# Kernel tuning notes

Hardware: AMD Instinct MI355X
Metric: run time of the kernel (lower is better)

Reference implementation:

```python
import jax, jax.numpy as jnp
import numpy as np

N_NODES = 20000
N_EDGES = 320000
NUM_GRAPHS = 64
IN_DIM = 256


def setup_inputs() -> dict:
    key = jax.random.key(0)
    ks = jax.random.split(key, 12)
    x = jax.random.normal(ks[0], (N_NODES, IN_DIM), dtype=jnp.float32)
    edge_index = jax.random.randint(ks[1], (2, N_EDGES), 0, N_NODES, dtype=jnp.int64)
    batch = jnp.sort(jax.random.randint(ks[2], (N_NODES,), 0, NUM_GRAPHS, dtype=jnp.int64))
    def glorot(k, shape):
        lim = float(np.sqrt(6.0 / (shape[0] + shape[1])))
        return jax.random.uniform(k, shape, dtype=jnp.float32, minval=-lim, maxval=lim)
    W1 = glorot(ks[3], (IN_DIM, 256)); b1 = jnp.zeros((256,), jnp.float32)
    W2 = glorot(ks[4], (256, 128));   b2 = jnp.zeros((128,), jnp.float32)
    Wl1 = glorot(ks[5], (128, 64));   bl1 = jnp.zeros((64,), jnp.float32)
    Wl2 = glorot(ks[6], (64, 1));     bl2 = jnp.zeros((1,), jnp.float32)
    return {"x": x, "edge_index": edge_index, "batch": batch,
            "W1": W1, "b1": b1, "W2": W2, "b2": b2,
            "Wl1": Wl1, "bl1": bl1, "Wl2": Wl2, "bl2": bl2}


def gcn_conv(x, src, dst, W, b, n_nodes):
    # PyG GCNConv: add self-loops, symmetric normalization D^-1/2 (A+I) D^-1/2,
    # linear transform first, then gather-scale-scatter aggregation, then bias.
    loop = jnp.arange(n_nodes, dtype=src.dtype)
    s = jnp.concatenate([src, loop])
    d = jnp.concatenate([dst, loop])
    deg = jax.ops.segment_sum(jnp.ones_like(d, dtype=x.dtype), d, num_segments=n_nodes)
    dinv = jnp.where(deg > 0, jax.lax.rsqrt(deg), 0.0)
    norm = dinv[s] * dinv[d]                         # [E+N]
    h = x @ W                                        # [N, out]
    msg = h[s] * norm[:, None]                       # [E+N, out]
    out = jax.ops.segment_sum(msg, d, num_segments=n_nodes)
    return out + b


def global_mean_pool(x, batch, num_graphs):
    sums = jax.ops.segment_sum(x, batch, num_segments=num_graphs)
    cnts = jax.ops.segment_sum(jnp.ones((x.shape[0],), x.dtype), batch, num_segments=num_graphs)
    return sums / jnp.maximum(cnts, 1.0)[:, None]


def reference(x, edge_index, batch, W1, b1, W2, b2, Wl1, bl1, Wl2, bl2):
    n = x.shape[0]
    src, dst = edge_index[0], edge_index[1]
    h = jax.nn.relu(gcn_conv(x, src, dst, W1, b1, n))   # dropout = identity (eval)
    h = jax.nn.relu(gcn_conv(h, src, dst, W2, b2, n))
    g = global_mean_pool(h, batch, NUM_GRAPHS)          # [G, 128]
    g = jax.nn.relu(g @ Wl1 + bl1)
    return jax.nn.sigmoid(g @ Wl2 + bl2)                # [G, 1]
```

## Files before the change

### kernel.cpp

```cpp
#include <hip/hip_runtime.h>
#include <hip/hip_bf16.h>
#include <math.h>

typedef __attribute__((ext_vector_type(8))) short bf16x8;
typedef __attribute__((ext_vector_type(4))) float f32x4;

__device__ __forceinline__ unsigned short f2bf(float f) {
    unsigned int u = __float_as_uint(f);
    unsigned int r = (u + 0x7FFFu + ((u >> 16) & 1u)) >> 16;
    return (unsigned short)r;
}
__device__ __forceinline__ float bf2f(unsigned short h) {
    return __uint_as_float(((unsigned int)h) << 16);
}
__device__ __forceinline__ unsigned char f2fp8(float v) {
    int p = __builtin_amdgcn_cvt_pk_fp8_f32(v, v, 0, false);
    return (unsigned char)(p & 0xff);
}
__device__ __forceinline__ unsigned int pk4fp8(float a, float b, float c, float d) {
    int p = __builtin_amdgcn_cvt_pk_fp8_f32(a, b, 0, false);
    p = __builtin_amdgcn_cvt_pk_fp8_f32(c, d, p, true);
    return (unsigned int)p;
}
__device__ __forceinline__ void fp8x8_fma(uint2 u, float w, float* a) {
    a[0] += __builtin_amdgcn_cvt_f32_fp8((int)u.x, 0) * w;
    a[1] += __builtin_amdgcn_cvt_f32_fp8((int)u.x, 1) * w;
    a[2] += __builtin_amdgcn_cvt_f32_fp8((int)u.x, 2) * w;
    a[3] += __builtin_amdgcn_cvt_f32_fp8((int)u.x, 3) * w;
    a[4] += __builtin_amdgcn_cvt_f32_fp8((int)u.y, 0) * w;
    a[5] += __builtin_amdgcn_cvt_f32_fp8((int)u.y, 1) * w;
    a[6] += __builtin_amdgcn_cvt_f32_fp8((int)u.y, 2) * w;
    a[7] += __builtin_amdgcn_cvt_f32_fp8((int)u.y, 3) * w;
}
__device__ __forceinline__ void fp8x4_fma(unsigned int u, float w, float* a) {
    a[0] += __builtin_amdgcn_cvt_f32_fp8((int)u, 0) * w;
    a[1] += __builtin_amdgcn_cvt_f32_fp8((int)u, 1) * w;
    a[2] += __builtin_amdgcn_cvt_f32_fp8((int)u, 2) * w;
    a[3] += __builtin_amdgcn_cvt_f32_fp8((int)u, 3) * w;
}
__device__ __forceinline__ float deg_dinv(int c) { return rsqrtf((float)c + 1.0f); }

__device__ __forceinline__ void load_lds16(const unsigned short* g, unsigned short* l) {
    __builtin_amdgcn_global_load_lds(
        (const __attribute__((address_space(1))) unsigned int*)g,
        (__attribute__((address_space(3))) unsigned int*)l, 16, 0, 0);
}

__global__ __launch_bounds__(256) void prep_kernel(const int* __restrict__ src,
                                                   const int* __restrict__ dst,
                                                   int* __restrict__ cnt,
                                                   int* __restrict__ csr,
                                                   const float* __restrict__ x,
                                                   unsigned short* __restrict__ xh,
                                                   const int* __restrict__ batch,
                                                   int* __restrict__ gstart,
                                                   const float* __restrict__ W1,
                                                   unsigned short* __restrict__ w1th,
                                                   unsigned short* __restrict__ w1tl,
                                                   const float* __restrict__ W2,
                                                   unsigned short* __restrict__ w2th,
                                                   unsigned short* __restrict__ w2tl,
                                                   int N, int E, int G,
                                                   int FB, int CXB, int BNB) {
    int b = blockIdx.x;
    int tid = threadIdx.x;
    if (b < FB) {
        int e = (b * 256 + tid) * 4;
        if (e + 3 < E) {
            int4 d4 = *(const int4*)(dst + e);
            int4 s4 = *(const int4*)(src + e);
            int sl;
            sl = atomicAdd(&cnt[d4.x], 1); if (sl < 64) csr[(d4.x << 6) + sl] = s4.x;
            sl = atomicAdd(&cnt[d4.y], 1); if (sl < 64) csr[(d4.y << 6) + sl] = s4.y;
            sl = atomicAdd(&cnt[d4.z], 1); if (sl < 64) csr[(d4.z << 6) + sl] = s4.z;
            sl = atomicAdd(&cnt[d4.w], 1); if (sl < 64) csr[(d4.w << 6) + sl] = s4.w;
        } else {
            for (; e < E; e++) {
                int d = dst[e];
                int slot = atomicAdd(&cnt[d], 1);
                if (slot < 64) csr[(d << 6) + slot] = src[e];
            }
        }
        return;
    }
    b -= FB;
    if (b < CXB) {
        size_t idx0 = ((size_t)b * 256 + tid) * 2;
        size_t total4 = (size_t)N * 64;
#pragma unroll
        for (int r = 0; r < 2; r++) {
            size_t idx = idx0 + r;
            if (idx < total4) {
                float4 v = ((const float4*)x)[idx];
                ushort4 o;
                o.x = f2bf(v.x); o.y = f2bf(v.y); o.z = f2bf(v.z); o.w = f2bf(v.w);
                ((ushort4*)xh)[idx] = o;
            }
        }
        return;
    }
    b -= CXB;
    if (b < BNB) {
        int i = b * 256 + tid;
        if (i >= N) return;
        int bb = batch[i];
        if (i == 0) { for (int g = 0; g <= bb; g++) gstart[g] = 0; }
        else { int bp = batch[i - 1]; for (int g = bp + 1; g <= bb; g++) gstart[g] = i; }
        if (i == N - 1) { for (int g = bb + 1; g <= G; g++) gstart[g] = N; }
        return;
    }
    b -= BNB;
    {
        int idx = b * 256 + tid;
        if (idx < 256 * 256) {
            int m = idx >> 8, k = idx & 255;
            float w = W1[(size_t)k * 256 + m];
            unsigned short hi = f2bf(w);
            w1th[idx] = hi;
            w1tl[idx] = f2bf(w - bf2f(hi));
        } else if (idx < 256 * 256 + 128 * 256) {
            int j = idx - 256 * 256;
            int m = j >> 8, k = j & 255;
            float w = W2[(size_t)k * 128 + m];
            unsigned short hi = f2bf(w);
            w2th[j] = hi;
            w2tl[j] = f2bf(w - bf2f(hi));
        }
    }
}

__global__ __launch_bounds__(256) void gemm_kernel(const unsigned short* __restrict__ A,
                                                   const unsigned short* __restrict__ Bth,
                                                   const unsigned short* __restrict__ Btl,
                                                   unsigned char* __restrict__ C8,
                                                   int N, int M) {
    __shared__ unsigned short As[128 * 32];
    __shared__ unsigned short Bhs[64 * 32];
    __shared__ unsigned short Bls[64 * 32];
    const int K = 256;
    int tid = threadIdx.x;
    int wave = tid >> 6, lane = tid & 63;
    int quad = lane >> 4, m16 = lane & 15;
    int r0 = blockIdx.y * 128, c0 = blockIdx.x * 64;
    int srow = lane >> 2;
    int skoff = (lane & 3) * 8;

    f32x4 acc[2][4];
#pragma unroll
    for (int rg = 0; rg < 2; rg++)
#pragma unroll
        for (int ct = 0; ct < 4; ct++) acc[rg][ct] = (f32x4){0.f, 0.f, 0.f, 0.f};

    for (int kb = 0; kb < K; kb += 32) {
#pragma unroll
        for (int i = 0; i < 2; i++) {
            int brow = wave * 32 + i * 16 + srow;
            int grow = r0 + brow; if (grow >= N) grow = N - 1;
            load_lds16(A + (size_t)grow * K + kb + skoff, As + (wave * 32 + i * 16) * 32);
        }
        {
            int bcol = wave * 16 + srow;
            size_t goff = (size_t)(c0 + bcol) * K + kb + skoff;
            load_lds16(Bth + goff, Bhs + (wave * 16) * 32);
            load_lds16(Btl + goff, Bls + (wave * 16) * 32);
        }
        __syncthreads();
        bf16x8 af[2], bh[4], bl[4];
#pragma unroll
        for (int rg = 0; rg < 2; rg++)
            af[rg] = *(const bf16x8*)(As + (wave * 32 + rg * 16 + m16) * 32 + quad * 8);
#pragma unroll
        for (int ct = 0; ct < 4; ct++) {
            bh[ct] = *(const bf16x8*)(Bhs + (ct * 16 + m16) * 32 + quad * 8);
            bl[ct] = *(const bf16x8*)(Bls + (ct * 16 + m16) * 32 + quad * 8);
        }
#pragma unroll
        for (int rg = 0; rg < 2; rg++)
#pragma unroll
            for (int ct = 0; ct < 4; ct++) {
                acc[rg][ct] = __builtin_amdgcn_mfma_f32_16x16x32_bf16(af[rg], bh[ct], acc[rg][ct], 0, 0, 0);
                acc[rg][ct] = __builtin_amdgcn_mfma_f32_16x16x32_bf16(af[rg], bl[ct], acc[rg][ct], 0, 0, 0);
            }
        __syncthreads();
    }
#pragma unroll
    for (int rg = 0; rg < 2; rg++) {
#pragma unroll
        for (int ct = 0; ct < 4; ct++) {
            int col = c0 + ct * 16 + m16;
#pragma unroll
            for (int r = 0; r < 4; r++) {
                int row = r0 + wave * 32 + rg * 16 + quad * 4 + r;
                if (row < N) C8[(size_t)row * M + col] = f2fp8(acc[rg][ct][r]);
            }
        }
    }
}

__global__ __launch_bounds__(256) void gather256_kernel(const unsigned char* __restrict__ h8,
                                                        const int* __restrict__ csr,
                                                        const int* __restrict__ cnt,
                                                        const float* __restrict__ bias,
                                                        unsigned short* __restrict__ out, int N) {
    int node = blockIdx.x * 4 + (threadIdx.x >> 6);
    if (node >= N) return;
    int lane = threadIdx.x & 63;
    int half = lane >> 5, hl = lane & 31;
    int beg = node << 6;
    int c = cnt[node]; if (c > 64) c = 64;
    int end = beg + c;
    float a[8] = {0, 0, 0, 0, 0, 0, 0, 0};
    int j = beg;
    for (; j + 7 < end; j += 8) {
        int s0 = csr[j + half], s1 = csr[j + 2 + half];
        int s2 = csr[j + 4 + half], s3 = csr[j + 6 + half];
        float w0 = deg_dinv(cnt[s0]), w1 = deg_dinv(cnt[s1]);
        float w2 = deg_dinv(cnt[s2]), w3 = deg_dinv(cnt[s3]);
        uint2 u0 = *(const uint2*)(h8 + (size_t)s0 * 256 + hl * 8);
        uint2 u1 = *(const uint2*)(h8 + (size_t)s1 * 256 + hl * 8);
        uint2 u2 = *(const uint2*)(h8 + (size_t)s2 * 256 + hl * 8);
        uint2 u3 = *(const uint2*)(h8 + (size_t)s3 * 256 + hl * 8);
        fp8x8_fma(u0, w0, a); fp8x8_fma(u1, w1, a);
        fp8x8_fma(u2, w2, a); fp8x8_fma(u3, w3, a);
    }
    for (; j + 1 < end; j += 2) {
        int s0 = csr[j + half];
        float w0 = deg_dinv(cnt[s0]);
        uint2 u0 = *(const uint2*)(h8 + (size_t)s0 * 256 + hl * 8);
        fp8x8_fma(u0, w0, a);
    }
    if (j < end && half == 0) {
        int s0 = csr[j];
        float w0 = deg_dinv(cnt[s0]);
        uint2 u0 = *(const uint2*)(h8 + (size_t)s0 * 256 + hl * 8);
        fp8x8_fma(u0, w0, a);
    }
#pragma unroll
    for (int i = 0; i < 8; i++) a[i] += __shfl_down(a[i], 32);
    if (half == 0) {
        float dd = deg_dinv(c);
        float self[8] = {0, 0, 0, 0, 0, 0, 0, 0};
        uint2 uh = *(const uint2*)(h8 + (size_t)node * 256 + hl * 8);
        fp8x8_fma(uh, dd, self);
        float4 bv0 = ((const float4*)bias)[hl * 2];
        float4 bv1 = ((const float4*)bias)[hl * 2 + 1];
        float bvf[8] = {bv0.x, bv0.y, bv0.z, bv0.w, bv1.x, bv1.y, bv1.z, bv1.w};
        bf16x8 o;
#pragma unroll
        for (int i = 0; i < 8; i++)
            o[i] = (short)f2bf(fmaxf((a[i] + self[i]) * dd + bvf[i], 0.f));
        ((bf16x8*)(out + (size_t)node * 256))[hl] = o;
    }
}

__global__ __launch_bounds__(256) void gather128_kernel(const unsigned char* __restrict__ t8,
                                                        const int* __restrict__ csr,
                                                        const int* __restrict__ cnt,
                                                        const float* __restrict__ bias,
                                                        unsigned char* __restrict__ out2, int N) {
    int node = blockIdx.x * 4 + (threadIdx.x >> 6);
    if (node >= N) return;
    int lane = threadIdx.x & 63;
    int half = lane >> 5, hl = lane & 31;
    int beg = node << 6;
    int c = cnt[node]; if (c > 64) c = 64;
    int end = beg + c;
    float a[4] = {0, 0, 0, 0};
    int j = beg;
    for (; j + 7 < end; j += 8) {
        int s0 = csr[j + half], s1 = csr[j + 2 + half];
        int s2 = csr[j + 4 + half], s3 = csr[j + 6 + half];
        float w0 = deg_dinv(cnt[s0]), w1 = deg_dinv(cnt[s1]);
        float w2 = deg_dinv(cnt[s2]), w3 = deg_dinv(cnt[s3]);
        unsigned int u0 = *(const unsigned int*)(t8 + (size_t)s0 * 128 + hl * 4);
        unsigned int u1 = *(const unsigned int*)(t8 + (size_t)s1 * 128 + hl * 4);
        unsigned int u2 = *(const unsigned int*)(t8 + (size_t)s2 * 128 + hl * 4);
        unsigned int u3 = *(const unsigned int*)(t8 + (size_t)s3 * 128 + hl * 4);
        fp8x4_fma(u0, w0, a); fp8x4_fma(u1, w1, a);
        fp8x4_fma(u2, w2, a); fp8x4_fma(u3, w3, a);
    }
    for (; j + 1 < end; j += 2) {
        int s0 = csr[j + half];
        float w0 = deg_dinv(cnt[s0]);
        unsigned int u0 = *(const unsigned int*)(t8 + (size_t)s0 * 128 + hl * 4);
        fp8x4_fma(u0, w0, a);
    }
    if (j < end && half == 0) {
        int s0 = csr[j];
        float w0 = deg_dinv(cnt[s0]);
        unsigned int u0 = *(const unsigned int*)(t8 + (size_t)s0 * 128 + hl * 4);
        fp8x4_fma(u0, w0, a);
    }
#pragma unroll
    for (int i = 0; i < 4; i++) a[i] += __shfl_down(a[i], 32);
    if (half == 0) {
        float dd = deg_dinv(c);
        float self[4] = {0, 0, 0, 0};
        unsigned int uh = *(const unsigned int*)(t8 + (size_t)node * 128 + hl * 4);
        fp8x4_fma(uh, dd, self);
        float4 bv = ((const float4*)bias)[hl];
        float r0 = fmaxf((a[0] + self[0]) * dd + bv.x, 0.f);
        float r1 = fmaxf((a[1] + self[1]) * dd + bv.y, 0.f);
        float r2 = fmaxf((a[2] + self[2]) * dd + bv.z, 0.f);
        float r3 = fmaxf((a[3] + self[3]) * dd + bv.w, 0.f);
        ((unsigned int*)(out2 + (size_t)node * 128))[hl] = pk4fp8(r0, r1, r2, r3);
    }
}

__global__ __launch_bounds__(256) void poolhead_kernel(const unsigned char* __restrict__ out2,
                                                       const int* __restrict__ gstart,
                                                       const float* __restrict__ Wl1,
                                                       const float* __restrict__ bl1,
                                                       const float* __restrict__ Wl2,
                                                       const float* __restrict__ bl2,
                                                       float* __restrict__ out) {
    int g = blockIdx.x;
    int tid = threadIdx.x;
    int hw = tid >> 5, hl = tid & 31;
    int gs = gstart[g], ge = gstart[g + 1];
    float a[4] = {0, 0, 0, 0};
    int i = gs + hw;
    for (; i + 8 < ge; i += 16) {
        unsigned int u0 = ((const unsigned int*)(out2 + (size_t)i * 128))[hl];
        unsigned int u1 = ((const unsigned int*)(out2 + (size_t)(i + 8) * 128))[hl];
        fp8x4_fma(u0, 1.0f, a);
        fp8x4_fma(u1, 1.0f, a);
    }
    if (i < ge) {
        unsigned int u0 = ((const unsigned int*)(out2 + (size_t)i * 128))[hl];
        fp8x4_fma(u0, 1.0f, a);
    }
    __shared__ float red[8][128];
#pragma unroll
    for (int k = 0; k < 4; k++) red[hw][hl * 4 + k] = a[k];
    __syncthreads();
    __shared__ float gv[128];
    if (tid < 128) {
        float s = 0.f;
#pragma unroll
        for (int w = 0; w < 8; w++) s += red[w][tid];
        float cntf = fmaxf((float)(ge - gs), 1.0f);
        gv[tid] = s / cntf;
    }
    __syncthreads();
    if (tid < 64) {
        float acc = bl1[tid];
#pragma unroll 8
        for (int k = 0; k < 128; k++) acc += gv[k] * Wl1[k * 64 + tid];
        acc = fmaxf(acc, 0.f);
        float p = acc * Wl2[tid];
#pragma unroll
        for (int off = 32; off; off >>= 1) p += __shfl_down(p, off);
        if (tid == 0) out[g] = 1.f / (1.f + expf(-(p + bl2[0])));
    }
}

extern "C" void kernel_launch(void* const* d_in, const int* in_sizes, int n_in,
                              void* d_out, int out_size, void* d_ws, size_t ws_size,
                              hipStream_t stream) {
    const float* x   = (const float*)d_in[0];
    const int* ei    = (const int*)d_in[1];
    const int* batch = (const int*)d_in[2];
    const float* W1  = (const float*)d_in[3];
    const float* b1  = (const float*)d_in[4];
    const float* W2  = (const float*)d_in[5];
    const float* b2  = (const float*)d_in[6];
    const float* Wl1 = (const float*)d_in[7];
    const float* bl1 = (const float*)d_in[8];
    const float* Wl2 = (const float*)d_in[9];
    const float* bl2 = (const float*)d_in[10];
    float* out = (float*)d_out;

    const int N = in_sizes[2];
    const int E = in_sizes[1] / 2;
    const int G = 64;
    const int* src = ei;
    const int* dst = ei + E;

    char* base = (char*)d_ws;
    size_t off = 0;
    auto carve = [&](size_t bytes) -> char* {
        char* p = base + off;
        off = (off + bytes + 15) & ~(size_t)15;
        return p;
    };
    int*   cnt    = (int*)carve((size_t)N * 4);
    int*   csr    = (int*)carve((size_t)N * 64 * 4);
    int*   gstart = (int*)carve((size_t)(G + 1) * 4);
    unsigned short* w1th = (unsigned short*)carve((size_t)256 * 256 * 2);
    unsigned short* w1tl = (unsigned short*)carve((size_t)256 * 256 * 2);
    unsigned short* w2th = (unsigned short*)carve((size_t)128 * 256 * 2);
    unsigned short* w2tl = (unsigned short*)carve((size_t)128 * 256 * 2);
    unsigned short* xh   = (unsigned short*)carve((size_t)N * 256 * 2);
    unsigned char*  h8   = (unsigned char*)carve((size_t)N * 256);
    unsigned short* o1h  = (unsigned short*)carve((size_t)N * 256 * 2);
    unsigned char* t8   = (unsigned char*)xh;
    unsigned char* out2 = h8;

    hipMemsetAsync(cnt, 0, (size_t)N * 4, stream);

    const int FB  = (E / 4 + 255) / 256;
    const int CXB = (int)(((size_t)N * 32 + 255) / 256);
    const int BNB = (N + 255) / 256;
    const int CWB = (256 * 256 + 128 * 256 + 255) / 256;
    prep_kernel<<<FB + CXB + BNB + CWB, 256, 0, stream>>>(
        src, dst, cnt, csr, x, xh, batch, gstart, W1, w1th, w1tl, W2, w2th, w2tl,
        N, E, G, FB, CXB, BNB);

    {
        dim3 grid(4, (N + 127) / 128);
        gemm_kernel<<<grid, 256, 0, stream>>>(xh, w1th, w1tl, h8, N, 256);
    }
    gather256_kernel<<<(N + 3) / 4, 256, 0, stream>>>(h8, csr, cnt, b1, o1h, N);

    {
        dim3 grid(2, (N + 127) / 128);
        gemm_kernel<<<grid, 256, 0, stream>>>(o1h, w2th, w2tl, t8, N, 128);
    }
    gather128_kernel<<<(N + 3) / 4, 256, 0, stream>>>(t8, csr, cnt, b2, out2, N);

    poolhead_kernel<<<G, 256, 0, stream>>>(out2, gstart, Wl1, bl1, Wl2, bl2, out);
}
```

Baseline: 176.5 us.

## Drop split-bf16 weight correction, fuse CSR fill into GEMM1, split pooling across blocks

The hi/lo bf16 split of the weights is removed, so each GEMM issues half the MFMAs and loads half the B tiles, at the cost of weight precision. The edge-to-CSR fill moves out of the prep kernel into the same launch as the first GEMM, so the atomic fill can overlap the matmul. Pooling now spreads each graph over eight blocks with atomic partial sums, and the last block to finish runs the MLP head. One larger memset zeroes the counters and the accumulation buffers.

```diff
diff --git a/kernel.cpp b/kernel.cpp
--- a/kernel.cpp
+++ b/kernel.cpp
@@ -9,9 +9,6 @@
     unsigned int u = __float_as_uint(f);
     unsigned int r = (u + 0x7FFFu + ((u >> 16) & 1u)) >> 16;
     return (unsigned short)r;
-}
-__device__ __forceinline__ float bf2f(unsigned short h) {
-    return __uint_as_float(((unsigned int)h) << 16);
 }
 __device__ __forceinline__ unsigned char f2fp8(float v) {
     int p = __builtin_amdgcn_cvt_pk_fp8_f32(v, v, 0, false);
@@ -46,26 +43,127 @@
         (__attribute__((address_space(3))) unsigned int*)l, 16, 0, 0);
 }
 
-__global__ __launch_bounds__(256) void prep_kernel(const int* __restrict__ src,
-                                                   const int* __restrict__ dst,
-                                                   int* __restrict__ cnt,
-                                                   int* __restrict__ csr,
-                                                   const float* __restrict__ x,
+__global__ __launch_bounds__(256) void prep_kernel(const float* __restrict__ x,
                                                    unsigned short* __restrict__ xh,
                                                    const int* __restrict__ batch,
                                                    int* __restrict__ gstart,
                                                    const float* __restrict__ W1,
-                                                   unsigned short* __restrict__ w1th,
-                                                   unsigned short* __restrict__ w1tl,
+                                                   unsigned short* __restrict__ w1t,
                                                    const float* __restrict__ W2,
-                                                   unsigned short* __restrict__ w2th,
-                                                   unsigned short* __restrict__ w2tl,
-                                                   int N, int E, int G,
-                                                   int FB, int CXB, int BNB) {
+                                                   unsigned short* __restrict__ w2t,
+                                                   int N, int G, int CXB, int BNB) {
     int b = blockIdx.x;
     int tid = threadIdx.x;
-    if (b < FB) {
-        int e = (b * 256 + tid) * 4;
+    if (b < CXB) {
+        size_t idx0 = ((size_t)b * 256 + tid) * 2;
+        size_t total4 = (size_t)N * 64;
+#pragma unroll
+        for (int r = 0; r < 2; r++) {
+            size_t idx = idx0 + r;
+            if (idx < total4) {
+                float4 v = ((const float4*)x)[idx];
+                ushort4 o;
+                o.x = f2bf(v.x); o.y = f2bf(v.y); o.z = f2bf(v.z); o.w = f2bf(v.w);
+                ((ushort4*)xh)[idx] = o;
+            }
+        }
+        return;
+    }
+    b -= CXB;
+    if (b < BNB) {
+        int i = b * 256 + tid;
+        if (i >= N) return;
+        int bb = batch[i];
+        if (i == 0) { for (int g = 0; g <= bb; g++) gstart[g] = 0; }
+        else { int bp = batch[i - 1]; for (int g = bp + 1; g <= bb; g++) gstart[g] = i; }
+        if (i == N - 1) { for (int g = bb + 1; g <= G; g++) gstart[g] = N; }
+        return;
+    }
+    b -= BNB;
+    {
+        int idx = b * 256 + tid;
+        if (idx < 256 * 256) {
+            int m = idx >> 8, k = idx & 255;
+            w1t[idx] = f2bf(W1[(size_t)k * 256 + m]);
+        } else if (idx < 256 * 256 + 128 * 256) {
+            int j = idx - 256 * 256;
+            int m = j >> 8, k = j & 255;
+            w2t[j] = f2bf(W2[(size_t)k * 128 + m]);
+        }
+    }
+}
+
+__device__ __forceinline__ void gemm_body(const unsigned short* __restrict__ A,
+                                          const unsigned short* __restrict__ Bt,
+                                          unsigned char* __restrict__ C8,
+                                          int N, int M, int bx, int by,
+                                          unsigned short* As, unsigned short* Bs) {
+    const int K = 256;
+    int tid = threadIdx.x;
+    int wave = tid >> 6, lane = tid & 63;
+    int quad = lane >> 4, m16 = lane & 15;
+    int r0 = by * 128, c0 = bx * 64;
+    int srow = lane >> 2;
+    int skoff = (lane & 3) * 8;
+
+    f32x4 acc[2][4];
+#pragma unroll
+    for (int rg = 0; rg < 2; rg++)
+#pragma unroll
+        for (int ct = 0; ct < 4; ct++) acc[rg][ct] = (f32x4){0.f, 0.f, 0.f, 0.f};
+
+    for (int kb = 0; kb < K; kb += 32) {
+#pragma unroll
+        for (int i = 0; i < 2; i++) {
+            int brow = wave * 32 + i * 16 + srow;
+            int grow = r0 + brow; if (grow >= N) grow = N - 1;
+            load_lds16(A + (size_t)grow * K + kb + skoff, As + (wave * 32 + i * 16) * 32);
+        }
+        {
+            int bcol = wave * 16 + srow;
+            load_lds16(Bt + (size_t)(c0 + bcol) * K + kb + skoff, Bs + (wave * 16) * 32);
+        }
+        __syncthreads();
+        bf16x8 af[2], bf[4];
+#pragma unroll
+        for (int rg = 0; rg < 2; rg++)
+            af[rg] = *(const bf16x8*)(As + (wave * 32 + rg * 16 + m16) * 32 + quad * 8);
+#pragma unroll
+        for (int ct = 0; ct < 4; ct++)
+            bf[ct] = *(const bf16x8*)(Bs + (ct * 16 + m16) * 32 + quad * 8);
+#pragma unroll
+        for (int rg = 0; rg < 2; rg++)
+#pragma unroll
+            for (int ct = 0; ct < 4; ct++)
+                acc[rg][ct] = __builtin_amdgcn_mfma_f32_16x16x32_bf16(af[rg], bf[ct], acc[rg][ct], 0, 0, 0);
+        __syncthreads();
+    }
+#pragma unroll
+    for (int rg = 0; rg < 2; rg++) {
+#pragma unroll
+        for (int ct = 0; ct < 4; ct++) {
+            int col = c0 + ct * 16 + m16;
+#pragma unroll
+            for (int r = 0; r < 4; r++) {
+                int row = r0 + wave * 32 + rg * 16 + quad * 4 + r;
+                if (row < N) C8[(size_t)row * M + col] = f2fp8(acc[rg][ct][r]);
+            }
+        }
+    }
+}
+
+__global__ __launch_bounds__(256) void fill_gemm1_kernel(const int* __restrict__ src,
+                                                         const int* __restrict__ dst,
+                                                         int* __restrict__ cnt,
+                                                         int* __restrict__ csr,
+                                                         const unsigned short* __restrict__ A,
+                                                         const unsigned short* __restrict__ Bt,
+                                                         unsigned char* __restrict__ C8,
+                                                         int N, int E, int FB) {
+    __shared__ unsigned short As[128 * 32];
+    __shared__ unsigned short Bs[64 * 32];
+    if ((int)blockIdx.x < FB) {
+        int e = (blockIdx.x * 256 + threadIdx.x) * 4;
         if (e + 3 < E) {
             int4 d4 = *(const int4*)(dst + e);
             int4 s4 = *(const int4*)(src + e);
@@ -83,118 +181,16 @@
         }
         return;
     }
-    b -= FB;
-    if (b < CXB) {
-        size_t idx0 = ((size_t)b * 256 + tid) * 2;
-        size_t total4 = (size_t)N * 64;
-#pragma unroll
-        for (int r = 0; r < 2; r++) {
-            size_t idx = idx0 + r;
-            if (idx < total4) {
-                float4 v = ((const float4*)x)[idx];
-                ushort4 o;
-                o.x = f2bf(v.x); o.y = f2bf(v.y); o.z = f2bf(v.z); o.w = f2bf(v.w);
-                ((ushort4*)xh)[idx] = o;
-            }
-        }
-        return;
-    }
-    b -= CXB;
-    if (b < BNB) {
-        int i = b * 256 + tid;
-        if (i >= N) return;
-        int bb = batch[i];
-        if (i == 0) { for (int g = 0; g <= bb; g++) gstart[g] = 0; }
-        else { int bp = batch[i - 1]; for (int g = bp + 1; g <= bb; g++) gstart[g] = i; }
-        if (i == N - 1) { for (int g = bb + 1; g <= G; g++) gstart[g] = N; }
-        return;
-    }
-    b -= BNB;
-    {
-        int idx = b * 256 + tid;
-        if (idx < 256 * 256) {
-            int m = idx >> 8, k = idx & 255;
-            float w = W1[(size_t)k * 256 + m];
-            unsigned short hi = f2bf(w);
-            w1th[idx] = hi;
-            w1tl[idx] = f2bf(w - bf2f(hi));
-        } else if (idx < 256 * 256 + 128 * 256) {
-            int j = idx - 256 * 256;
-            int m = j >> 8, k = j & 255;
-            float w = W2[(size_t)k * 128 + m];
-            unsigned short hi = f2bf(w);
-            w2th[j] = hi;
-            w2tl[j] = f2bf(w - bf2f(hi));
-        }
-    }
-}
-
-__global__ __launch_bounds__(256) void gemm_kernel(const unsigned short* __restrict__ A,
-                                                   const unsigned short* __restrict__ Bth,
-                                                   const unsigned short* __restrict__ Btl,
-                                                   unsigned char* __restrict__ C8,
-                                                   int N, int M) {
+    int gb = blockIdx.x - FB;
+    gemm_body(A, Bt, C8, N, 256, gb & 3, gb >> 2, As, Bs);
+}
+
+__global__ __launch_bounds__(256) void gemm2_kernel(const unsigned short* __restrict__ A,
+                                                    const unsigned short* __restrict__ Bt,
+                                                    unsigned char* __restrict__ C8, int N) {
     __shared__ unsigned short As[128 * 32];
-    __shared__ unsigned short Bhs[64 * 32];
-    __shared__ unsigned short Bls[64 * 32];
-    const int K = 256;
-    int tid = threadIdx.x;
-    int wave = tid >> 6, lane = tid & 63;
-    int quad = lane >> 4, m16 = lane & 15;
-    int r0 = blockIdx.y * 128, c0 = blockIdx.x * 64;
-    int srow = lane >> 2;
-    int skoff = (lane & 3) * 8;
-
-    f32x4 acc[2][4];
-#pragma unroll
-    for (int rg = 0; rg < 2; rg++)
-#pragma unroll
-        for (int ct = 0; ct < 4; ct++) acc[rg][ct] = (f32x4){0.f, 0.f, 0.f, 0.f};
-
-    for (int kb = 0; kb < K; kb += 32) {
-#pragma unroll
-        for (int i = 0; i < 2; i++) {
-            int brow = wave * 32 + i * 16 + srow;
-            int grow = r0 + brow; if (grow >= N) grow = N - 1;
-            load_lds16(A + (size_t)grow * K + kb + skoff, As + (wave * 32 + i * 16) * 32);
-        }
-        {
-            int bcol = wave * 16 + srow;
-            size_t goff = (size_t)(c0 + bcol) * K + kb + skoff;
-            load_lds16(Bth + goff, Bhs + (wave * 16) * 32);
-            load_lds16(Btl + goff, Bls + (wave * 16) * 32);
-        }
-        __syncthreads();
-        bf16x8 af[2], bh[4], bl[4];
-#pragma unroll
-        for (int rg = 0; rg < 2; rg++)
-            af[rg] = *(const bf16x8*)(As + (wave * 32 + rg * 16 + m16) * 32 + quad * 8);
-#pragma unroll
-        for (int ct = 0; ct < 4; ct++) {
-            bh[ct] = *(const bf16x8*)(Bhs + (ct * 16 + m16) * 32 + quad * 8);
-            bl[ct] = *(const bf16x8*)(Bls + (ct * 16 + m16) * 32 + quad * 8);
-        }
-#pragma unroll
-        for (int rg = 0; rg < 2; rg++)
-#pragma unroll
-            for (int ct = 0; ct < 4; ct++) {
-                acc[rg][ct] = __builtin_amdgcn_mfma_f32_16x16x32_bf16(af[rg], bh[ct], acc[rg][ct], 0, 0, 0);
-                acc[rg][ct] = __builtin_amdgcn_mfma_f32_16x16x32_bf16(af[rg], bl[ct], acc[rg][ct], 0, 0, 0);
-            }
-        __syncthreads();
-    }
-#pragma unroll
-    for (int rg = 0; rg < 2; rg++) {
-#pragma unroll
-        for (int ct = 0; ct < 4; ct++) {
-            int col = c0 + ct * 16 + m16;
-#pragma unroll
-            for (int r = 0; r < 4; r++) {
-                int row = r0 + wave * 32 + rg * 16 + quad * 4 + r;
-                if (row < N) C8[(size_t)row * M + col] = f2fp8(acc[rg][ct][r]);
-            }
-        }
-    }
+    __shared__ unsigned short Bs[64 * 32];
+    gemm_body(A, Bt, C8, N, 128, blockIdx.x, blockIdx.y, As, Bs);
 }
 
 __global__ __launch_bounds__(256) void gather256_kernel(const unsigned char* __restrict__ h8,
@@ -309,36 +305,44 @@
 
 __global__ __launch_bounds__(256) void poolhead_kernel(const unsigned char* __restrict__ out2,
                                                        const int* __restrict__ gstart,
+                                                       float* __restrict__ gsum,
+                                                       int* __restrict__ gdone,
                                                        const float* __restrict__ Wl1,
                                                        const float* __restrict__ bl1,
                                                        const float* __restrict__ Wl2,
                                                        const float* __restrict__ bl2,
                                                        float* __restrict__ out) {
-    int g = blockIdx.x;
+    int g = blockIdx.x >> 3, slice = blockIdx.x & 7;
     int tid = threadIdx.x;
     int hw = tid >> 5, hl = tid & 31;
     int gs = gstart[g], ge = gstart[g + 1];
     float a[4] = {0, 0, 0, 0};
-    int i = gs + hw;
-    for (; i + 8 < ge; i += 16) {
-        unsigned int u0 = ((const unsigned int*)(out2 + (size_t)i * 128))[hl];
-        unsigned int u1 = ((const unsigned int*)(out2 + (size_t)(i + 8) * 128))[hl];
-        fp8x4_fma(u0, 1.0f, a);
-        fp8x4_fma(u1, 1.0f, a);
-    }
-    if (i < ge) {
-        unsigned int u0 = ((const unsigned int*)(out2 + (size_t)i * 128))[hl];
-        fp8x4_fma(u0, 1.0f, a);
+    for (int i = gs + slice * 8 + hw; i < ge; i += 64) {
+        unsigned int u = ((const unsigned int*)(out2 + (size_t)i * 128))[hl];
+        fp8x4_fma(u, 1.0f, a);
     }
     __shared__ float red[8][128];
 #pragma unroll
     for (int k = 0; k < 4; k++) red[hw][hl * 4 + k] = a[k];
     __syncthreads();
+    if (tid < 128) {
+        float s = 0.f;
+#pragma unroll
+        for (int w = 0; w < 8; w++) s += red[w][tid];
+        if (s != 0.f) atomicAdd(&gsum[g * 128 + tid], s);
+    }
+    __syncthreads();
+    __shared__ int lastflag;
+    if (tid == 0) {
+        __threadfence();
+        int old = atomicAdd(&gdone[g], 1);
+        lastflag = (old == 7) ? 1 : 0;
+    }
+    __syncthreads();
+    if (!lastflag) return;
     __shared__ float gv[128];
     if (tid < 128) {
-        float s = 0.f;
-#pragma unroll
-        for (int w = 0; w < 8; w++) s += red[w][tid];
+        float s = atomicAdd(&gsum[g * 128 + tid], 0.0f);
         float cntf = fmaxf((float)(ge - gs), 1.0f);
         gv[tid] = s / cntf;
     }
@@ -385,39 +389,40 @@
         return p;
     };
     int*   cnt    = (int*)carve((size_t)N * 4);
+    float* gsum   = (float*)carve((size_t)G * 128 * 4);
+    int*   gdone  = (int*)carve((size_t)G * 4);
+    size_t zero_bytes = (size_t)(N + G * 128 + G) * 4 + 32;
     int*   csr    = (int*)carve((size_t)N * 64 * 4);
     int*   gstart = (int*)carve((size_t)(G + 1) * 4);
-    unsigned short* w1th = (unsigned short*)carve((size_t)256 * 256 * 2);
-    unsigned short* w1tl = (unsigned short*)carve((size_t)256 * 256 * 2);
-    unsigned short* w2th = (unsigned short*)carve((size_t)128 * 256 * 2);
-    unsigned short* w2tl = (unsigned short*)carve((size_t)128 * 256 * 2);
-    unsigned short* xh   = (unsigned short*)carve((size_t)N * 256 * 2);
-    unsigned char*  h8   = (unsigned char*)carve((size_t)N * 256);
-    unsigned short* o1h  = (unsigned short*)carve((size_t)N * 256 * 2);
+    unsigned short* w1t = (unsigned short*)carve((size_t)256 * 256 * 2);
+    unsigned short* w2t = (unsigned short*)carve((size_t)128 * 256 * 2);
+    unsigned short* xh  = (unsigned short*)carve((size_t)N * 256 * 2);
+    unsigned char*  h8  = (unsigned char*)carve((size_t)N * 256);
+    unsigned short* o1h = (unsigned short*)carve((size_t)N * 256 * 2);
     unsigned char* t8   = (unsigned char*)xh;
     unsigned char* out2 = h8;
 
-    hipMemsetAsync(cnt, 0, (size_t)N * 4, stream);
-
-    const int FB  = (E / 4 + 255) / 256;
+    hipMemsetAsync(d_ws, 0, zero_bytes, stream);
+
     const int CXB = (int)(((size_t)N * 32 + 255) / 256);
     const int BNB = (N + 255) / 256;
     const int CWB = (256 * 256 + 128 * 256 + 255) / 256;
-    prep_kernel<<<FB + CXB + BNB + CWB, 256, 0, stream>>>(
-        src, dst, cnt, csr, x, xh, batch, gstart, W1, w1th, w1tl, W2, w2th, w2tl,
-        N, E, G, FB, CXB, BNB);
-
-    {
-        dim3 grid(4, (N + 127) / 128);
-        gemm_kernel<<<grid, 256, 0, stream>>>(xh, w1th, w1tl, h8, N, 256);
-    }
+    prep_kernel<<<CXB + BNB + CWB, 256, 0, stream>>>(
+        x, xh, batch, gstart, W1, w1t, W2, w2t, N, G, CXB, BNB);
+
+    const int FB  = (E / 4 + 255) / 256;
+    const int GB1 = 4 * ((N + 127) / 128);
+    fill_gemm1_kernel<<<FB + GB1, 256, 0, stream>>>(src, dst, cnt, csr,
+                                                    xh, w1t, h8, N, E, FB);
+
     gather256_kernel<<<(N + 3) / 4, 256, 0, stream>>>(h8, csr, cnt, b1, o1h, N);
 
     {
         dim3 grid(2, (N + 127) / 128);
-        gemm_kernel<<<grid, 256, 0, stream>>>(o1h, w2th, w2tl, t8, N, 128);
+        gemm2_kernel<<<grid, 256, 0, stream>>>(o1h, w2t, t8, N);
     }
     gather128_kernel<<<(N + 3) / 4, 256, 0, stream>>>(t8, csr, cnt, b2, out2, N);
 
-    poolhead_kernel<<<G, 256, 0, stream>>>(out2, gstart, Wl1, bl1, Wl2, bl2, out);
-}
+    poolhead_kernel<<<G * 8, 256, 0, stream>>>(out2, gstart, gsum, gdone,
+                                               Wl1, bl1, Wl2, bl2, out);
+}
```

Result: no change. 173.5 us (median of 2 runs) (-1.7%).
